# Kernel tuning notes

Measured on AMD Instinct MI355X. Metric: run time of the kernel, lower is better.

The kernel has to match this reference:

```python
import jax, jax.numpy as jnp
import numpy as np
from jax import lax

B, CEN, CDE, H, W = 4, 256, 256, 64, 64   # de is (B,CDE,H,W); en is (B,CEN,2H,2W)
EMB, K, SCALE = 64, 5, 2
DN = ('NCHW', 'OIHW', 'NCHW')


def conv2d(x, w, b=None, pad=0):
    y = lax.conv_general_dilated(x, w, (1, 1), [(pad, pad), (pad, pad)], dimension_numbers=DN)
    return y if b is None else y + b[None, :, None, None]


def up2(x):
    # F.interpolate(scale_factor=2) default mode='nearest'
    return jnp.repeat(jnp.repeat(x, 2, axis=2), 2, axis=3)


def carafe(de, kernels, k, scale):
    # de: (B,C,H,W); kernels: (B,k*k,H*scale,W*scale), softmax-normalized over dim 1
    b, c, h, w = de.shape
    pad = k // 2
    dep = jnp.pad(de, ((0, 0), (0, 0), (pad, pad), (pad, pad)))
    # (B, C, k*k, H, W): all k*k shifted views of de (zero-padded borders)
    patches = jnp.stack([dep[:, :, dy:dy + h, dx:dx + w]
                         for dy in range(k) for dx in range(k)], axis=2)
    # each output pixel (i,j) reuses the window at source (i//scale, j//scale)
    ker = kernels.reshape(b, k * k, h, scale, w, scale)
    out = jnp.einsum('bkhxwy,bckhw->bchxwy', ker, patches)
    return out.reshape(b, c, h * scale, w * scale)


def xavier_uniform(key, shape):
    fan_out = shape[0] * shape[2] * shape[3]
    fan_in = shape[1] * shape[2] * shape[3]
    limit = float(np.sqrt(6.0 / (fan_in + fan_out)))
    return jax.random.uniform(key, shape, jnp.float32, -limit, limit)


def setup_inputs() -> dict:
    key = jax.random.key(0)
    ks = jax.random.split(key, 7)
    return {
        'en': jax.random.normal(ks[0], (B, CEN, 2 * H, 2 * W), jnp.float32),
        'de': jax.random.normal(ks[1], (B, CDE, H, W), jnp.float32),
        'w_gate': xavier_uniform(ks[2], (1, CDE, 1, 1)),
        'b_gate': jnp.zeros((1,), jnp.float32),
        'w_cen': xavier_uniform(ks[3], (EMB, CEN, 1, 1)),
        'b_cen': jnp.zeros((EMB,), jnp.float32),
        'w_cde': xavier_uniform(ks[4], (EMB, CDE, 1, 1)),
        'w_ce': xavier_uniform(ks[5], (K * K, EMB, 3, 3)),
        'b_ce': jnp.zeros((K * K,), jnp.float32),
    }


def reference(en, de, w_gate, b_gate, w_cen, b_cen, w_cde, w_ce, b_ce):
    # GateGenerator: sigmoid(interpolate(conv1x1(de), x2))
    gate = jax.nn.sigmoid(up2(conv2d(de, w_gate, b_gate)))
    # SemiShift: shared 3x3 content encoder on compressed en and upsampled compressed de
    enc = conv2d(en, w_cen, b_cen)
    dec = conv2d(de, w_cde)          # no bias
    logits = conv2d(enc, w_ce, b_ce, pad=1) + up2(conv2d(dec, w_ce, b_ce, pad=1))
    kernels = jax.nn.softmax(logits, axis=1)
    return gate * en + (1.0 - gate) * carafe(de, kernels, K, SCALE)
```

## Files before the change

kernel.cpp:

```cpp
#include <hip/hip_runtime.h>
#include <math.h>

#define BB 4
#define C 256
#define H 64
#define W 64
#define HW 4096
#define HO 128
#define WO 128
#define HWO 16384
#define EMB 64

typedef __bf16 bf16x8 __attribute__((ext_vector_type(8)));
typedef __bf16 bf16x4 __attribute__((ext_vector_type(4)));
typedef float  f32x4  __attribute__((ext_vector_type(4)));

__device__ __forceinline__ f32x4 mfma16(bf16x8 a, bf16x8 b, f32x4 c) {
    return __builtin_amdgcn_mfma_f32_16x16x32_bf16(a, b, c, 0, 0, 0);
}

__global__ void k_prep2(const float* __restrict__ w_cen,
                        const float* __restrict__ w_cde,
                        const float* __restrict__ w_gate,
                        const float* __restrict__ w_ce,
                        __bf16* __restrict__ wbf_cen,
                        __bf16* __restrict__ wdec5,
                        __bf16* __restrict__ w3) {
    for (int idx = blockIdx.x * blockDim.x + threadIdx.x; idx < 16384;
         idx += gridDim.x * blockDim.x)
        wbf_cen[idx] = (__bf16)w_cen[idx];
    for (int idx = blockIdx.x * blockDim.x + threadIdx.x; idx < 20480;
         idx += gridDim.x * blockDim.x) {
        int c = idx & 255, m = (idx >> 8) & 15;
        float v;
        if (idx < 16384) v = w_cde[idx];
        else             v = (m == 0) ? w_gate[c] : 0.f;
        wdec5[idx] = (__bf16)v;
    }
    for (int idx = blockIdx.x * blockDim.x + threadIdx.x; idx < 18432;
         idx += gridDim.x * blockDim.x) {
        int e = idx & 63;
        int m = (idx >> 6) & 15;
        int mt = (idx >> 10) & 1;
        int tap = idx >> 11;
        int q = mt * 16 + m;
        int dy = tap / 3, dx = tap % 3;
        w3[idx] = (q < 25) ? (__bf16)w_ce[((q * EMB + e) * 3 + dy) * 3 + dx]
                           : (__bf16)0.0f;
    }
}

__global__ __launch_bounds__(256) void k_gemm1(
        const float* __restrict__ en, const float* __restrict__ de,
        const __bf16* __restrict__ wbf_cen, const __bf16* __restrict__ wdec5,
        const float* __restrict__ b_cen, const float* __restrict__ b_gate,
        __bf16* __restrict__ enc_t, __bf16* __restrict__ dec_t,
        float* __restrict__ gate_lr) {
    __shared__ float xs[2][32][136];
    int t = threadIdx.x;
    int w = t >> 6, lane = t & 63;
    int n = lane & 15, q = lane >> 4;
    bool isenc = blockIdx.x < 512;
    const float* X; const __bf16* Wt; __bf16* Y; int plane, px0, b;
    if (isenc) {
        int blk = blockIdx.x; b = blk >> 7; px0 = (blk & 127) << 7;
        X = en + (size_t)b * C * HWO; plane = HWO; Wt = wbf_cen;
        Y = enc_t + (size_t)b * HWO * EMB;
    } else {
        int blk = blockIdx.x - 512; b = blk >> 5; px0 = (blk & 31) << 7;
        X = de + (size_t)b * C * HW; plane = HW; Wt = wdec5;
        Y = dec_t + (size_t)b * HW * EMB;
    }
    int scc = t >> 5;
    int sp4 = (t & 31) << 2;
    float4 pre[4];
    #pragma unroll
    for (int i = 0; i < 4; i++)
        pre[i] = *(const float4*)(X + (size_t)(i * 8 + scc) * plane + px0 + sp4);
    #pragma unroll
    for (int i = 0; i < 4; i++)
        *(float4*)(&xs[0][i * 8 + scc][sp4]) = pre[i];
    __syncthreads();

    f32x4 acc[4][2] = {};
    f32x4 accg[2] = {};
    for (int kc = 0; kc < 8; kc++) {
        int cur = kc & 1;
        if (kc < 7) {
            int c1 = (kc + 1) * 32;
            #pragma unroll
            for (int i = 0; i < 4; i++)
                pre[i] = *(const float4*)(X + (size_t)(c1 + i * 8 + scc) * plane
                                          + px0 + sp4);
        }
        int c0 = kc * 32;
        bf16x8 af[4];
        #pragma unroll
        for (int mt = 0; mt < 4; mt++)
            af[mt] = *(const bf16x8*)(Wt + (size_t)(mt * 16 + n) * C + c0 + q * 8);
        bf16x8 bv[2];
        #pragma unroll
        for (int nt = 0; nt < 2; nt++) {
            int px = w * 32 + nt * 16 + n;
            #pragma unroll
            for (int j = 0; j < 8; j++)
                bv[nt][j] = (__bf16)xs[cur][q * 8 + j][px];
        }
        #pragma unroll
        for (int mt = 0; mt < 4; mt++) {
            acc[mt][0] = mfma16(af[mt], bv[0], acc[mt][0]);
            acc[mt][1] = mfma16(af[mt], bv[1], acc[mt][1]);
        }
        if (!isenc) {
            bf16x8 ag = *(const bf16x8*)(Wt + (size_t)(64 + n) * C + c0 + q * 8);
            accg[0] = mfma16(ag, bv[0], accg[0]);
            accg[1] = mfma16(ag, bv[1], accg[1]);
        }
        if (kc < 7) {
            #pragma unroll
            for (int i = 0; i < 4; i++)
                *(float4*)(&xs[cur ^ 1][i * 8 + scc][sp4]) = pre[i];
        }
        __syncthreads();
    }

    #pragma unroll
    for (int nt = 0; nt < 2; nt++) {
        int gpx = px0 + w * 32 + nt * 16 + n;
        #pragma unroll
        for (int mt = 0; mt < 4; mt++) {
            int e0 = mt * 16 + q * 4;
            bf16x4 ov;
            #pragma unroll
            for (int r = 0; r < 4; r++) {
                float bias = isenc ? b_cen[e0 + r] : 0.f;
                ov[r] = (__bf16)(acc[mt][nt][r] + bias);
            }
            *(bf16x4*)(Y + (size_t)gpx * EMB + e0) = ov;
        }
        if (!isenc && q == 0)
            gate_lr[b * HW + gpx] =
                1.f / (1.f + __expf(-(accg[nt][0] + b_gate[0])));
    }
}

__global__ __launch_bounds__(256) void k_conv3m(
        const __bf16* __restrict__ enc_t, const __bf16* __restrict__ dec_t,
        const __bf16* __restrict__ w3, const float* __restrict__ b_ce,
        float* __restrict__ tmp1, float* __restrict__ tmp2) {
    __shared__ __bf16 sfr[8 * 3 * 66 * 8];
    int t = threadIdx.x;
    int w = t >> 6, lane = t & 63;
    int n = lane & 15, q = lane >> 4;
    bool hi = blockIdx.x < 1024;
    const __bf16* src; float* dst; int b, y, width, plane, x0;
    if (hi) {
        int blk = blockIdx.x; b = blk >> 8; int r = blk & 255;
        y = r >> 1; x0 = (r & 1) * 64;
        width = WO; plane = HWO;
        src = enc_t + (size_t)b * HWO * EMB; dst = tmp1;
    } else {
        int blk = blockIdx.x - 1024; b = blk >> 6; y = blk & 63; x0 = 0;
        width = W; plane = HW;
        src = dec_t + (size_t)b * HW * EMB; dst = tmp2;
    }
    bf16x8 zf;
    #pragma unroll
    for (int j = 0; j < 8; j++) zf[j] = (__bf16)0.0f;
    for (int idx = t; idx < 1584; idx += 256) {
        int f = idx & 7;
        int rem = idx >> 3;
        int xloc = rem % 66, row = rem / 66;
        int yy = y + row - 1, xg = x0 - 1 + xloc;
        bf16x8 v = zf;
        if ((unsigned)yy < (unsigned)width && (unsigned)xg < (unsigned)width)
            v = *(const bf16x8*)(src + ((size_t)yy * width + xg) * EMB + f * 8);
        *(bf16x8*)(sfr + (((f * 3) + row) * 66 + xloc) * 8) = v;
    }
    __syncthreads();

    int x = w * 16 + n;
    f32x4 acc[2] = {};
    #pragma unroll
    for (int row = 0; row < 3; row++) {
        #pragma unroll
        for (int dx = 0; dx < 3; dx++) {
            int tap = row * 3 + dx;
            #pragma unroll
            for (int kc = 0; kc < 2; kc++) {
                bf16x8 bv = *(const bf16x8*)(
                    sfr + ((((kc * 4 + q) * 3) + row) * 66 + x + dx) * 8);
                #pragma unroll
                for (int mt = 0; mt < 2; mt++) {
                    bf16x8 av = *(const bf16x8*)(
                        w3 + ((tap * 2 + mt) * 16 + n) * EMB + kc * 32 + q * 8);
                    acc[mt] = mfma16(av, bv, acc[mt]);
                }
            }
        }
    }
    #pragma unroll
    for (int mt = 0; mt < 2; mt++) {
        #pragma unroll
        for (int r = 0; r < 4; r++) {
            int m = mt * 16 + q * 4 + r;
            if (m < 25)
                dst[((size_t)(b * 25 + m)) * plane + y * width + x0 + x] =
                    acc[mt][r] + b_ce[m];
        }
    }
}

__global__ __launch_bounds__(256) void k_softmax(
        const float* __restrict__ tmp1, const float* __restrict__ tmp2,
        float* __restrict__ kbuf) {
    __shared__ float red[4][64];
    int t = threadIdx.x;
    int tx = t & 63, qg = t >> 6;
    int gp = blockIdx.x * 64 + tx;
    int b = gp >> 14, p = gp & 16383;
    int i = p >> 7, j = p & 127;
    int pl = (i >> 1) * W + (j >> 1);
    int q0 = qg * 7;
    int nq = (qg < 3) ? 7 : 4;
    float l[7];
    float mx = -1e30f;
    for (int iq = 0; iq < nq; iq++) {
        int qq = q0 + iq;
        l[iq] = tmp1[((size_t)(b * 25 + qq) << 14) + p]
              + tmp2[((size_t)(b * 25 + qq) << 12) + pl];
        mx = fmaxf(mx, l[iq]);
    }
    red[qg][tx] = mx;
    __syncthreads();
    mx = fmaxf(fmaxf(red[0][tx], red[1][tx]), fmaxf(red[2][tx], red[3][tx]));
    float s = 0.f;
    for (int iq = 0; iq < nq; iq++) { l[iq] = __expf(l[iq] - mx); s += l[iq]; }
    __syncthreads();
    red[qg][tx] = s;
    __syncthreads();
    s = red[0][tx] + red[1][tx] + red[2][tx] + red[3][tx];
    float inv = 1.f / s;
    float* kb = kbuf + (size_t)gp * 28;
    for (int iq = 0; iq < nq; iq++) kb[q0 + iq] = l[iq] * inv;
    if (qg == 3) { kb[25] = 0.f; kb[26] = 0.f; kb[27] = 0.f; }
}

#define NCH 16
__global__ __launch_bounds__(256) void k_final(
        const float* __restrict__ en, const float* __restrict__ de,
        const float* __restrict__ kbuf, const float* __restrict__ gate_lr,
        float* __restrict__ out) {
    __shared__ float sde[NCH][12][36];
    int t = threadIdx.x;
    int x0 = (blockIdx.x & 1) * 32, y0 = (blockIdx.x >> 1) * 8;
    int c0 = blockIdx.y * NCH;
    int b = blockIdx.z;

    const float* dbase = de + ((size_t)b * C + c0) * HW;
    for (int idx = t; idx < NCH * 432; idx += 256) {
        int c = idx / 432, rem = idx % 432;
        int row = rem / 36, col = rem % 36;
        int yy = y0 - 2 + row, xx = x0 - 2 + col;
        float v = 0.f;
        if ((unsigned)yy < (unsigned)H && (unsigned)xx < (unsigned)W)
            v = dbase[(size_t)c * HW + yy * W + xx];
        sde[c][row][col] = v;
    }

    int tx = t & 31, ty = t >> 5;
    int yl = y0 + ty, xl = x0 + tx;
    float kern[4][25];
    #pragma unroll
    for (int hp = 0; hp < 4; hp++) {
        int ii = 2 * yl + (hp >> 1), jj = 2 * xl + (hp & 1);
        const float* kb = kbuf + ((size_t)b * HWO + ii * WO + jj) * 28;
        #pragma unroll
        for (int v = 0; v < 6; v++)
            *(float4*)&kern[hp][v * 4] = *(const float4*)(kb + v * 4);
        kern[hp][24] = kb[24];
    }
    float g = gate_lr[b * HW + yl * W + xl];
    float gm = 1.f - g;
    __syncthreads();

    const float* ebase = en + ((size_t)b * C + c0) * HWO + (2 * yl) * WO + 2 * xl;
    float* obase = out + ((size_t)b * C + c0) * HWO + (2 * yl) * WO + 2 * xl;
    #pragma unroll 2
    for (int c = 0; c < NCH; c++) {
        float a0 = 0.f, a1 = 0.f, a2 = 0.f, a3 = 0.f;
        #pragma unroll
        for (int dy = 0; dy < 5; dy++) {
            #pragma unroll
            for (int dx = 0; dx < 5; dx++) {
                float v = sde[c][ty + dy][tx + dx];
                int k = dy * 5 + dx;
                a0 += kern[0][k] * v;
                a1 += kern[1][k] * v;
                a2 += kern[2][k] * v;
                a3 += kern[3][k] * v;
            }
        }
        size_t cc = (size_t)c * HWO;
        float2 e0 = *(const float2*)(ebase + cc);
        float2 e1 = *(const float2*)(ebase + cc + WO);
        float2 o0, o1;
        o0.x = g * e0.x + gm * a0;  o0.y = g * e0.y + gm * a1;
        o1.x = g * e1.x + gm * a2;  o1.y = g * e1.y + gm * a3;
        *(float2*)(obase + cc) = o0;
        *(float2*)(obase + cc + WO) = o1;
    }
}

extern "C" void kernel_launch(void* const* d_in, const int* in_sizes, int n_in,
                              void* d_out, int out_size, void* d_ws, size_t ws_size,
                              hipStream_t stream) {
    const float* en     = (const float*)d_in[0];
    const float* de     = (const float*)d_in[1];
    const float* w_gate = (const float*)d_in[2];
    const float* b_gate = (const float*)d_in[3];
    const float* w_cen  = (const float*)d_in[4];
    const float* b_cen  = (const float*)d_in[5];
    const float* w_cde  = (const float*)d_in[6];
    const float* w_ce   = (const float*)d_in[7];
    const float* b_ce   = (const float*)d_in[8];
    float* out = (float*)d_out;

    __bf16* wsb     = (__bf16*)d_ws;
    __bf16* wbf_cen = wsb;
    __bf16* wdec5   = wbf_cen + 16384;
    __bf16* w3      = wdec5 + 20480;
    __bf16* enc_t   = w3 + 18432;
    __bf16* dec_t   = enc_t + 4194304;
    float* wsf     = (float*)((char*)d_ws + (size_t)(16384 + 20480 + 18432
                              + 4194304 + 1048576) * 2);
    float* tmp1    = wsf;
    float* tmp2    = tmp1 + 1638400;
    float* gate_lr = tmp2 + 409600;
    float* kbuf    = gate_lr + 16384;

    k_prep2<<<80, 256, 0, stream>>>(w_cen, w_cde, w_gate, w_ce,
                                    wbf_cen, wdec5, w3);
    k_gemm1<<<640, 256, 0, stream>>>(en, de, wbf_cen, wdec5, b_cen, b_gate,
                                     enc_t, dec_t, gate_lr);
    k_conv3m<<<1280, 256, 0, stream>>>(enc_t, dec_t, w3, b_ce, tmp1, tmp2);
    k_softmax<<<1024, 256, 0, stream>>>(tmp1, tmp2, kbuf);
    k_final<<<dim3(16, 16, 4), 256, 0, stream>>>(en, de, kbuf, gate_lr, out);
}
```

Baseline: 234.2 us.

## Fuse softmax into CARAFE final kernel and halve per-thread output pixels

New measurement: 414.0 us. +76.8%, slower.

```diff
diff --git a/kernel.cpp b/kernel.cpp
--- a/kernel.cpp
+++ b/kernel.cpp
@@ -211,55 +211,20 @@
     }
 }
 
-__global__ __launch_bounds__(256) void k_softmax(
+#define NCH 16
+__global__ __launch_bounds__(256, 5) void k_final(
+        const float* __restrict__ en, const float* __restrict__ de,
         const float* __restrict__ tmp1, const float* __restrict__ tmp2,
-        float* __restrict__ kbuf) {
-    __shared__ float red[4][64];
+        const float* __restrict__ gate_lr, float* __restrict__ out) {
+    __shared__ float sde[NCH][8][36];
     int t = threadIdx.x;
-    int tx = t & 63, qg = t >> 6;
-    int gp = blockIdx.x * 64 + tx;
-    int b = gp >> 14, p = gp & 16383;
-    int i = p >> 7, j = p & 127;
-    int pl = (i >> 1) * W + (j >> 1);
-    int q0 = qg * 7;
-    int nq = (qg < 3) ? 7 : 4;
-    float l[7];
-    float mx = -1e30f;
-    for (int iq = 0; iq < nq; iq++) {
-        int qq = q0 + iq;
-        l[iq] = tmp1[((size_t)(b * 25 + qq) << 14) + p]
-              + tmp2[((size_t)(b * 25 + qq) << 12) + pl];
-        mx = fmaxf(mx, l[iq]);
-    }
-    red[qg][tx] = mx;
-    __syncthreads();
-    mx = fmaxf(fmaxf(red[0][tx], red[1][tx]), fmaxf(red[2][tx], red[3][tx]));
-    float s = 0.f;
-    for (int iq = 0; iq < nq; iq++) { l[iq] = __expf(l[iq] - mx); s += l[iq]; }
-    __syncthreads();
-    red[qg][tx] = s;
-    __syncthreads();
-    s = red[0][tx] + red[1][tx] + red[2][tx] + red[3][tx];
-    float inv = 1.f / s;
-    float* kb = kbuf + (size_t)gp * 28;
-    for (int iq = 0; iq < nq; iq++) kb[q0 + iq] = l[iq] * inv;
-    if (qg == 3) { kb[25] = 0.f; kb[26] = 0.f; kb[27] = 0.f; }
-}
-
-#define NCH 16
-__global__ __launch_bounds__(256) void k_final(
-        const float* __restrict__ en, const float* __restrict__ de,
-        const float* __restrict__ kbuf, const float* __restrict__ gate_lr,
-        float* __restrict__ out) {
-    __shared__ float sde[NCH][12][36];
-    int t = threadIdx.x;
-    int x0 = (blockIdx.x & 1) * 32, y0 = (blockIdx.x >> 1) * 8;
+    int x0 = (blockIdx.x & 1) * 32, y0 = (blockIdx.x >> 1) * 4;
     int c0 = blockIdx.y * NCH;
     int b = blockIdx.z;
 
     const float* dbase = de + ((size_t)b * C + c0) * HW;
-    for (int idx = t; idx < NCH * 432; idx += 256) {
-        int c = idx / 432, rem = idx % 432;
+    for (int idx = t; idx < NCH * 288; idx += 256) {
+        int c = idx / 288, rem = idx % 288;
         int row = rem / 36, col = rem % 36;
         int yy = y0 - 2 + row, xx = x0 - 2 + col;
         float v = 0.f;
@@ -268,47 +233,57 @@
         sde[c][row][col] = v;
     }
 
-    int tx = t & 31, ty = t >> 5;
+    int tx = t & 31;
+    int tyr = t >> 5;
+    int ty = tyr >> 1, r = tyr & 1;
     int yl = y0 + ty, xl = x0 + tx;
-    float kern[4][25];
-    #pragma unroll
-    for (int hp = 0; hp < 4; hp++) {
-        int ii = 2 * yl + (hp >> 1), jj = 2 * xl + (hp & 1);
-        const float* kb = kbuf + ((size_t)b * HWO + ii * WO + jj) * 28;
-        #pragma unroll
-        for (int v = 0; v < 6; v++)
-            *(float4*)&kern[hp][v * 4] = *(const float4*)(kb + v * 4);
-        kern[hp][24] = kb[24];
-    }
-    float g = gate_lr[b * HW + yl * W + xl];
-    float gm = 1.f - g;
+    int hrow = 2 * yl + r;
+    int p0 = hrow * WO + 2 * xl;
+    int pl = yl * W + xl;
+
+    float l0[25], l1[25];
+    const float* t1 = tmp1 + (((size_t)b * 25) << 14) + p0;
+    const float* t2 = tmp2 + (((size_t)b * 25) << 12) + pl;
+    float mx0 = -1e30f, mx1 = -1e30f;
+    #pragma unroll
+    for (int q = 0; q < 25; q++) {
+        float2 a = *(const float2*)(t1 + ((size_t)q << 14));
+        float cq = t2[(size_t)q << 12];
+        l0[q] = a.x + cq; l1[q] = a.y + cq;
+        mx0 = fmaxf(mx0, l0[q]); mx1 = fmaxf(mx1, l1[q]);
+    }
+    float s0 = 0.f, s1 = 0.f;
+    #pragma unroll
+    for (int q = 0; q < 25; q++) {
+        l0[q] = __expf(l0[q] - mx0); s0 += l0[q];
+        l1[q] = __expf(l1[q] - mx1); s1 += l1[q];
+    }
+    float g = gate_lr[b * HW + pl];
+    float gi0 = (1.f - g) / s0;
+    float gi1 = (1.f - g) / s1;
     __syncthreads();
 
-    const float* ebase = en + ((size_t)b * C + c0) * HWO + (2 * yl) * WO + 2 * xl;
-    float* obase = out + ((size_t)b * C + c0) * HWO + (2 * yl) * WO + 2 * xl;
+    const float* ebase = en + ((size_t)b * C + c0) * HWO + p0;
+    float* obase = out + ((size_t)b * C + c0) * HWO + p0;
     #pragma unroll 2
     for (int c = 0; c < NCH; c++) {
-        float a0 = 0.f, a1 = 0.f, a2 = 0.f, a3 = 0.f;
+        float a0 = 0.f, a1 = 0.f;
         #pragma unroll
         for (int dy = 0; dy < 5; dy++) {
             #pragma unroll
             for (int dx = 0; dx < 5; dx++) {
                 float v = sde[c][ty + dy][tx + dx];
                 int k = dy * 5 + dx;
-                a0 += kern[0][k] * v;
-                a1 += kern[1][k] * v;
-                a2 += kern[2][k] * v;
-                a3 += kern[3][k] * v;
+                a0 += l0[k] * v;
+                a1 += l1[k] * v;
             }
         }
         size_t cc = (size_t)c * HWO;
-        float2 e0 = *(const float2*)(ebase + cc);
-        float2 e1 = *(const float2*)(ebase + cc + WO);
-        float2 o0, o1;
-        o0.x = g * e0.x + gm * a0;  o0.y = g * e0.y + gm * a1;
-        o1.x = g * e1.x + gm * a2;  o1.y = g * e1.y + gm * a3;
-        *(float2*)(obase + cc) = o0;
-        *(float2*)(obase + cc + WO) = o1;
+        float2 e = *(const float2*)(ebase + cc);
+        float2 o;
+        o.x = g * e.x + gi0 * a0;
+        o.y = g * e.y + gi1 * a1;
+        *(float2*)(obase + cc) = o;
     }
 }
 
@@ -337,13 +312,12 @@
     float* tmp1    = wsf;
     float* tmp2    = tmp1 + 1638400;
     float* gate_lr = tmp2 + 409600;
-    float* kbuf    = gate_lr + 16384;
 
     k_prep2<<<80, 256, 0, stream>>>(w_cen, w_cde, w_gate, w_ce,
                                     wbf_cen, wdec5, w3);
     k_gemm1<<<640, 256, 0, stream>>>(en, de, wbf_cen, wdec5, b_cen, b_gate,
                                      enc_t, dec_t, gate_lr);
     k_conv3m<<<1280, 256, 0, stream>>>(enc_t, dec_t, w3, b_ce, tmp1, tmp2);
-    k_softmax<<<1024, 256, 0, stream>>>(tmp1, tmp2, kbuf);
-    k_final<<<dim3(16, 16, 4), 256, 0, stream>>>(en, de, kbuf, gate_lr, out);
-}
+    k_final<<<dim3(32, 16, 4), 256, 0, stream>>>(en, de, tmp1, tmp2,
+                                                 gate_lr, out);
+}
```
